# Optimization experiments

Hardware: AMD Instinct MI355X
Metric: run time of the kernel (lower is better)

## Reference

```python
import jax, jax.numpy as jnp
import numpy as np

N = 100_000
E = 1_600_000
H = 128
L = 3
EPS = 1e-5


def setup_inputs() -> dict:
    key = jax.random.key(0)
    ks = jax.random.split(key, 8)
    x = jax.random.normal(ks[0], (N, H), dtype=jnp.float32)
    edge_index = jax.random.randint(ks[1], (2, E), 0, N, dtype=jnp.int64)
    edge_weight = jax.random.uniform(ks[2], (E,), dtype=jnp.float32)
    # per-layer params (all layers are H->H since in_dim == hidden)
    s = 1.0 / np.sqrt(H)
    lin_neigh_w = jax.random.uniform(ks[3], (L, H, H), minval=-s, maxval=s, dtype=jnp.float32)
    lin_root_w = jax.random.uniform(ks[4], (L, H, H), minval=-s, maxval=s, dtype=jnp.float32)
    lin_root_b = jax.random.uniform(ks[5], (L, H), minval=-s, maxval=s, dtype=jnp.float32)
    ln_w = jnp.ones((L, H), dtype=jnp.float32)
    ln_b = jnp.zeros((L, H), dtype=jnp.float32)
    return {"x": x, "edge_index": edge_index, "edge_weight": edge_weight,
            "lin_neigh_w": lin_neigh_w, "lin_root_w": lin_root_w,
            "lin_root_b": lin_root_b, "ln_w": ln_w, "ln_b": ln_b}


def _layer(h, src, dst, e_w, w_neigh, w_root, b_root, g, b):
    # message: m_ij = w_ij * x_j ; aggregate: scatter-add over dst, normalized by sum of weights
    msg = e_w[:, None] * h[src]                                    # [E, H]
    agg = jax.ops.segment_sum(msg, dst, num_segments=N)            # [N, H]
    sum_w = jnp.clip(jax.ops.segment_sum(e_w, dst, num_segments=N), 1.0, None)
    out = agg / sum_w[:, None]
    out = out @ w_neigh.T + h @ w_root.T + b_root                  # lin_neigh + lin_root
    out = jax.nn.relu(out)
    # per-node LayerNorm over feature dim
    mu = jnp.mean(out, axis=-1, keepdims=True)
    var = jnp.var(out, axis=-1, keepdims=True)
    out = (out - mu) * jax.lax.rsqrt(var + EPS) * g + b
    return out  # dropout: inference no-op


def reference(x, edge_index, edge_weight, lin_neigh_w, lin_root_w, lin_root_b, ln_w, ln_b):
    src, dst = edge_index[0], edge_index[1]
    h = x
    for l in range(L):
        h = _layer(h, src, dst, edge_weight, lin_neigh_w[l], lin_root_w[l],
                   lin_root_b[l], ln_w[l], ln_b[l])
    return h
```

## Files before the change

### kernel.cpp

```cpp
#include <hip/hip_runtime.h>

#define H 128
#define EPS 1e-5f
#define BCAP 6144

typedef __attribute__((ext_vector_type(8))) short short8;
typedef __attribute__((ext_vector_type(4))) float f32x4;

__device__ inline unsigned short f2bf(float f) {
    unsigned u = __builtin_bit_cast(unsigned, f);
    unsigned r = (u + 0x7fff + ((u >> 16) & 1)) >> 16;
    return (unsigned short)r;
}
__device__ inline float bf2f_lo(unsigned u) { return __builtin_bit_cast(float, u << 16); }
__device__ inline float bf2f_hi(unsigned u) { return __builtin_bit_cast(float, u & 0xffff0000u); }

__global__ void convert_kernel(const float* __restrict__ x, unsigned* __restrict__ hx, int n4) {
    int i = blockIdx.x * 256 + threadIdx.x;
    if (i >= n4) return;
    float4 v = reinterpret_cast<const float4*>(x)[i];
    unsigned p0 = (unsigned)f2bf(v.x) | ((unsigned)f2bf(v.y) << 16);
    unsigned p1 = (unsigned)f2bf(v.z) | ((unsigned)f2bf(v.w) << 16);
    reinterpret_cast<uint2*>(hx)[i] = make_uint2(p0, p1);
}

__global__ __launch_bounds__(256) void bhist_kernel(const int* __restrict__ dst,
                                                    int* __restrict__ ghist, int E, int NB) {
    __shared__ int hist[512];
    int t = threadIdx.x;
    for (int i = t; i < NB; i += 256) hist[i] = 0;
    __syncthreads();
    int base = blockIdx.x * 8192 + t;
#pragma unroll
    for (int k = 0; k < 32; ++k) {
        int e = base + k * 256;
        if (e < E) atomicAdd(&hist[dst[e] >> 8], 1);
    }
    __syncthreads();
    for (int i = t; i < NB; i += 256)
        if (hist[i]) atomicAdd(&ghist[i], hist[i]);
}

__global__ __launch_bounds__(512) void bscan_kernel(const int* __restrict__ ghist,
                                                    int* __restrict__ bucket_base,
                                                    int* __restrict__ cursor,
                                                    int* __restrict__ row_start,
                                                    int NB, int E, int N) {
    __shared__ int lds[512];
    int t = threadIdx.x;
    int v = (t < NB) ? ghist[t] : 0;
    lds[t] = v;
    __syncthreads();
    for (int off = 1; off < 512; off <<= 1) {
        int u = (t >= off) ? lds[t - off] : 0;
        __syncthreads();
        lds[t] += u;
        __syncthreads();
    }
    int excl = lds[t] - v;
    if (t < NB) {
        bucket_base[t] = excl;
        cursor[t] = excl;
    }
    if (t == 0) {
        bucket_base[NB] = E;
        row_start[N] = E;
    }
}

__global__ __launch_bounds__(1024) void bucketize_kernel(const int* __restrict__ src,
                                                         const int* __restrict__ dst,
                                                         const float* __restrict__ ew,
                                                         int* __restrict__ cursor,
                                                         int2* __restrict__ ee, int E, int NB) {
    __shared__ int hist[512];
    __shared__ int scn[512];
    __shared__ int gbase[512];
    __shared__ int2 stage[8192];
    int t = threadIdx.x;
    for (int i = t; i < NB; i += 1024) hist[i] = 0;
    __syncthreads();

    int e0 = blockIdx.x * 8192;
    int bb[8], rk[8], pk[8], wb[8];
#pragma unroll
    for (int k = 0; k < 8; ++k) {
        int e = e0 + t + k * 1024;
        if (e < E) {
            int s = src[e], d = dst[e];
            bb[k] = d >> 8;
            pk[k] = s | ((d & 255) << 17);
            wb[k] = __float_as_int(ew[e]);
            rk[k] = atomicAdd(&hist[bb[k]], 1);
        } else {
            bb[k] = -1;
        }
    }
    __syncthreads();
    if (t < 512) scn[t] = (t < NB) ? hist[t] : 0;
    __syncthreads();
    for (int off = 1; off < 512; off <<= 1) {
        int u = 0;
        if (t < 512 && t >= off) u = scn[t - off];
        __syncthreads();
        if (t < 512) scn[t] += u;
        __syncthreads();
    }
    for (int i = t; i < NB; i += 1024) {
        int c = hist[i];
        if (c > 0) gbase[i] = atomicAdd(&cursor[i], c);
    }
#pragma unroll
    for (int k = 0; k < 8; ++k) {
        if (bb[k] >= 0) {
            int start = scn[bb[k]] - hist[bb[k]];
            stage[start + rk[k]] = make_int2(pk[k], wb[k]);
        }
    }
    __syncthreads();
    int wv = t >> 6, ln = t & 63;
    for (int bk = wv; bk < NB; bk += 16) {
        int c = hist[bk];
        if (c == 0) continue;
        int s0 = scn[bk] - c;
        int gb = gbase[bk];
        for (int i = ln; i < c; i += 64) ee[gb + i] = stage[s0 + i];
    }
}

__global__ __launch_bounds__(256) void bsort_kernel(int2* __restrict__ ee,
                                                    const int* __restrict__ bucket_base,
                                                    int* __restrict__ row_start, int N) {
    __shared__ int cnts[256];
    __shared__ int scv[256];
    __shared__ int prefs[256];
    __shared__ int2 out[BCAP];
    int b = blockIdx.x;
    int base = bucket_base[b], endb = bucket_base[b + 1];
    int cnt = endb - base;
    int t = threadIdx.x;
    cnts[t] = 0;
    __syncthreads();
    for (int i = base + t; i < endb; i += 256) atomicAdd(&cnts[(ee[i].x >> 17) & 255], 1);
    __syncthreads();
    scv[t] = cnts[t];
    __syncthreads();
    for (int off = 1; off < 256; off <<= 1) {
        int u = (t >= off) ? scv[t - off] : 0;
        __syncthreads();
        scv[t] += u;
        __syncthreads();
    }
    int pref = scv[t] - cnts[t];
    prefs[t] = pref;
    int node = (b << 8) + t;
    if (node < N) row_start[node] = base + pref;
    __syncthreads();
    cnts[t] = 0;
    __syncthreads();
    for (int i = base + t; i < endb; i += 256) {
        int2 r = ee[i];
        int dl = (r.x >> 17) & 255;
        int rkk = atomicAdd(&cnts[dl], 1);
        int slot = prefs[dl] + rkk;
        if (slot < BCAP) out[slot] = make_int2(r.x & 0x1FFFF, r.y);
    }
    __syncthreads();
    for (int i = t; i < cnt; i += 256) ee[base + i] = out[i];
}

__global__ __launch_bounds__(256) void agg_kernel(const unsigned short* __restrict__ hx,
                                                  const int* __restrict__ row_start,
                                                  const int2* __restrict__ ee,
                                                  unsigned short* __restrict__ aggb, int N) {
    int t = threadIdx.x;
    int node = blockIdx.x * 4 + (t >> 6);
    if (node >= N) return;
    int lane = t & 63, half = lane >> 5, jb = lane & 31;
    float a0 = 0.f, a1 = 0.f, a2 = 0.f, a3 = 0.f, sw = 0.f;
    int rs = row_start[node], re = row_start[node + 1];
    int i = rs + half;
    for (; i + 2 < re; i += 4) {
        int2 ea = ee[i], eb = ee[i + 2];
        uint2 ua = reinterpret_cast<const uint2*>(hx + (size_t)ea.x * H)[jb];
        uint2 ub = reinterpret_cast<const uint2*>(hx + (size_t)eb.x * H)[jb];
        float wa = __int_as_float(ea.y), wbv = __int_as_float(eb.y);
        a0 = fmaf(wa, bf2f_lo(ua.x), a0); a1 = fmaf(wa, bf2f_hi(ua.x), a1);
        a2 = fmaf(wa, bf2f_lo(ua.y), a2); a3 = fmaf(wa, bf2f_hi(ua.y), a3);
        a0 = fmaf(wbv, bf2f_lo(ub.x), a0); a1 = fmaf(wbv, bf2f_hi(ub.x), a1);
        a2 = fmaf(wbv, bf2f_lo(ub.y), a2); a3 = fmaf(wbv, bf2f_hi(ub.y), a3);
        sw += wa + wbv;
    }
    for (; i < re; i += 2) {
        int2 ea = ee[i];
        uint2 ua = reinterpret_cast<const uint2*>(hx + (size_t)ea.x * H)[jb];
        float wa = __int_as_float(ea.y);
        a0 = fmaf(wa, bf2f_lo(ua.x), a0); a1 = fmaf(wa, bf2f_hi(ua.x), a1);
        a2 = fmaf(wa, bf2f_lo(ua.y), a2); a3 = fmaf(wa, bf2f_hi(ua.y), a3);
        sw += wa;
    }
    a0 += __shfl_xor(a0, 32);
    a1 += __shfl_xor(a1, 32);
    a2 += __shfl_xor(a2, 32);
    a3 += __shfl_xor(a3, 32);
    sw += __shfl_xor(sw, 32);
    sw = sw < 1.f ? 1.f : sw;
    float inv = 1.f / sw;
    float fl = half ? a2 : a0;
    float fh = half ? a3 : a1;
    unsigned p = (unsigned)f2bf(fl * inv) | ((unsigned)f2bf(fh * inv) << 16);
    reinterpret_cast<unsigned*>(aggb + (size_t)node * H)[2 * jb + half] = p;
}

__global__ __launch_bounds__(256, 2) void gemm_ln_mfma(
    const unsigned short* __restrict__ aggb, const unsigned short* __restrict__ hx,
    const float* __restrict__ Wn, const float* __restrict__ Wr,
    const float* __restrict__ br, const float* __restrict__ g,
    const float* __restrict__ b, unsigned short* __restrict__ hout,
    float* __restrict__ outf, int final_layer, int N) {
    __shared__ short8 Bfl[4096];

    int t = threadIdx.x;
    int w = t >> 6, lane = t & 63;
    int Mbase = blockIdx.x * 256;

#pragma unroll
    for (int it = 0; it < 16; ++it) {
        int f = it * 4 + w;
        int kt = f >> 3, nb = f & 7;
        int n = nb * 16 + (lane & 15);
        int kk = (kt & 3) * 32 + (lane >> 4) * 8;
        const float* wp = ((kt < 4) ? Wn : Wr) + (size_t)n * H + kk;
        float4 wa = *reinterpret_cast<const float4*>(wp);
        float4 wb = *reinterpret_cast<const float4*>(wp + 4);
        short8 sv;
        sv[0] = (short)f2bf(wa.x); sv[1] = (short)f2bf(wa.y);
        sv[2] = (short)f2bf(wa.z); sv[3] = (short)f2bf(wa.w);
        sv[4] = (short)f2bf(wb.x); sv[5] = (short)f2bf(wb.y);
        sv[6] = (short)f2bf(wb.z); sv[7] = (short)f2bf(wb.w);
        Bfl[f * 64 + lane] = sv;
    }
    __syncthreads();

    int lrow = lane & 15, lk = lane >> 4;
    const char* aggp = (const char*)aggb;
    const char* hp = (const char*)hx;
    size_t rb[4];
#pragma unroll
    for (int mf = 0; mf < 4; ++mf) {
        int r = Mbase + w * 64 + mf * 16 + lrow;
        r = r < N ? r : N - 1;
        rb[mf] = (size_t)r * 256;
    }

    f32x4 acc[4][8];
#pragma unroll
    for (int mf = 0; mf < 4; ++mf)
#pragma unroll
        for (int nb = 0; nb < 8; ++nb) acc[mf][nb] = (f32x4){0.f, 0.f, 0.f, 0.f};

#pragma unroll
    for (int kt = 0; kt < 8; ++kt) {
        const char* base = (kt < 4) ? aggp : hp;
        int off = (kt & 3) * 64 + lk * 16;
        short8 bf[8];
#pragma unroll
        for (int nb = 0; nb < 8; ++nb) bf[nb] = Bfl[(kt * 8 + nb) * 64 + lane];
#pragma unroll
        for (int mf = 0; mf < 4; ++mf) {
            short8 av = *reinterpret_cast<const short8*>(base + rb[mf] + off);
#pragma unroll
            for (int nb = 0; nb < 8; ++nb)
                acc[mf][nb] = __builtin_amdgcn_mfma_f32_16x16x32_bf16(av, bf[nb], acc[mf][nb], 0, 0, 0);
        }
    }

    int col0 = lane & 15, rq = lane >> 4;
    float bias[8], gg[8], bbv[8];
#pragma unroll
    for (int nb = 0; nb < 8; ++nb) {
        int c = col0 + nb * 16;
        bias[nb] = br[c];
        gg[nb] = g[c];
        bbv[nb] = b[c];
    }
#pragma unroll
    for (int mf = 0; mf < 4; ++mf) {
#pragma unroll
        for (int reg = 0; reg < 4; ++reg) {
            float v[8];
            float s = 0.f, q = 0.f;
#pragma unroll
            for (int nb = 0; nb < 8; ++nb) {
                float u = acc[mf][nb][reg] + bias[nb];
                u = fmaxf(u, 0.f);
                v[nb] = u;
                s += u;
                q = fmaf(u, u, q);
            }
#pragma unroll
            for (int off = 1; off < 16; off <<= 1) {
                s += __shfl_xor(s, off);
                q += __shfl_xor(q, off);
            }
            float mu = s * (1.f / 128.f);
            float var = q * (1.f / 128.f) - mu * mu;
            float inv = rsqrtf(var + EPS);
            int grow = Mbase + w * 64 + mf * 16 + rq * 4 + reg;
            if (grow < N) {
                if (final_layer) {
#pragma unroll
                    for (int nb = 0; nb < 8; ++nb)
                        outf[(size_t)grow * H + col0 + nb * 16] = (v[nb] - mu) * inv * gg[nb] + bbv[nb];
                } else {
#pragma unroll
                    for (int nb = 0; nb < 8; ++nb)
                        hout[(size_t)grow * H + col0 + nb * 16] = f2bf((v[nb] - mu) * inv * gg[nb] + bbv[nb]);
                }
            }
        }
    }
}

static inline size_t alignup(size_t x) { return (x + 255) & ~(size_t)255; }

extern "C" void kernel_launch(void* const* d_in, const int* in_sizes, int n_in,
                              void* d_out, int out_size, void* d_ws, size_t ws_size,
                              hipStream_t stream) {
    const float* x  = (const float*)d_in[0];
    const int*   ei = (const int*)d_in[1];
    const float* ew = (const float*)d_in[2];
    const float* Wn = (const float*)d_in[3];
    const float* Wr = (const float*)d_in[4];
    const float* br = (const float*)d_in[5];
    const float* g  = (const float*)d_in[6];
    const float* bb = (const float*)d_in[7];
    float* out = (float*)d_out;

    int N = in_sizes[0] / H;
    int E = in_sizes[2];
    const int* src = ei;
    const int* dst = ei + E;
    int NB = (N + 255) >> 8;

    char* ws = (char*)d_ws;
    size_t off = 0;
    int* ghist = (int*)(ws + off);         off = alignup(off + sizeof(int) * 512);
    int* bucket_base = (int*)(ws + off);   off = alignup(off + sizeof(int) * 513);
    int* cursor = (int*)(ws + off);        off = alignup(off + sizeof(int) * 512);
    int* row_start = (int*)(ws + off);     off = alignup(off + sizeof(int) * ((size_t)N + 1));
    int2* ee = (int2*)(ws + off);          off = alignup(off + sizeof(int2) * (size_t)E);
    unsigned short* aggb = (unsigned short*)(ws + off); off = alignup(off + 2ull * N * H);
    unsigned short* hx = (unsigned short*)(ws + off);   off = alignup(off + 2ull * N * H);

    int eblocks = (E + 8191) / 8192;

    hipMemsetAsync(ghist, 0, sizeof(int) * 512, stream);
    bhist_kernel<<<eblocks, 256, 0, stream>>>(dst, ghist, E, NB);
    bscan_kernel<<<1, 512, 0, stream>>>(ghist, bucket_base, cursor, row_start, NB, E, N);
    bucketize_kernel<<<eblocks, 1024, 0, stream>>>(src, dst, ew, cursor, ee, E, NB);
    bsort_kernel<<<NB, 256, 0, stream>>>(ee, bucket_base, row_start, N);

    int n4 = N * H / 4;
    convert_kernel<<<(n4 + 255) / 256, 256, 0, stream>>>(x, (unsigned*)hx, n4);

    int gblocks = (N + 255) / 256;
    for (int l = 0; l < 3; ++l) {
        agg_kernel<<<(N + 3) / 4, 256, 0, stream>>>(hx, row_start, ee, aggb, N);
        gemm_ln_mfma<<<gblocks, 256, 0, stream>>>(
            aggb, hx,
            Wn + (size_t)l * H * H, Wr + (size_t)l * H * H, br + (size_t)l * H,
            g + (size_t)l * H, bb + (size_t)l * H,
            hx, out, (l == 2) ? 1 : 0, N);
    }
}
```

Before: 345.7 us.

## Switch activations to fp16 with packed half2 aggregation and prenormalized edge weights

Stores features in fp16 instead of bf16 and performs the neighbor aggregation with packed half2 FMAs, accumulating in fp16. Per-node weight-sum normalization moves into the CSR bucket-sort kernel, which writes each edge weight already divided by the clamped sum and duplicated as a half2. The aggregation loop is unrolled to four gathers per iteration, and the GEMM uses the f16 MFMA. This cuts conversion and FMA instruction count in the gather-bound aggregation, at the cost of fp16 accumulation error and overflow risk over many edges, plus a serial per-thread pass in the sort kernel.

```diff
diff --git a/kernel.cpp b/kernel.cpp
--- a/kernel.cpp
+++ b/kernel.cpp
@@ -1,26 +1,22 @@
 #include <hip/hip_runtime.h>
+#include <hip/hip_fp16.h>
 
 #define H 128
 #define EPS 1e-5f
 #define BCAP 6144
 
-typedef __attribute__((ext_vector_type(8))) short short8;
+typedef __attribute__((ext_vector_type(8))) _Float16 half8;
 typedef __attribute__((ext_vector_type(4))) float f32x4;
 
-__device__ inline unsigned short f2bf(float f) {
-    unsigned u = __builtin_bit_cast(unsigned, f);
-    unsigned r = (u + 0x7fff + ((u >> 16) & 1)) >> 16;
-    return (unsigned short)r;
-}
-__device__ inline float bf2f_lo(unsigned u) { return __builtin_bit_cast(float, u << 16); }
-__device__ inline float bf2f_hi(unsigned u) { return __builtin_bit_cast(float, u & 0xffff0000u); }
+__device__ inline __half2 u2h2(unsigned u) { return __builtin_bit_cast(__half2, u); }
+__device__ inline unsigned h22u(__half2 h) { return __builtin_bit_cast(unsigned, h); }
 
 __global__ void convert_kernel(const float* __restrict__ x, unsigned* __restrict__ hx, int n4) {
     int i = blockIdx.x * 256 + threadIdx.x;
     if (i >= n4) return;
     float4 v = reinterpret_cast<const float4*>(x)[i];
-    unsigned p0 = (unsigned)f2bf(v.x) | ((unsigned)f2bf(v.y) << 16);
-    unsigned p1 = (unsigned)f2bf(v.z) | ((unsigned)f2bf(v.w) << 16);
+    unsigned p0 = h22u(__floats2half2_rn(v.x, v.y));
+    unsigned p1 = h22u(__floats2half2_rn(v.z, v.w));
     reinterpret_cast<uint2*>(hx)[i] = make_uint2(p0, p1);
 }
 
@@ -166,6 +162,19 @@
         if (slot < BCAP) out[slot] = make_int2(r.x & 0x1FFFF, r.y);
     }
     __syncthreads();
+    {
+        int s0 = prefs[t], c = cnts[t];
+        float sw = 0.f;
+        for (int k = 0; k < c; ++k) sw += __int_as_float(out[s0 + k].y);
+        sw = sw < 1.f ? 1.f : sw;
+        float inv = 1.f / sw;
+        for (int k = 0; k < c; ++k) {
+            float w = __int_as_float(out[s0 + k].y) * inv;
+            unsigned hb = (unsigned)__half_as_ushort(__float2half(w));
+            out[s0 + k].y = (int)(hb | (hb << 16));
+        }
+    }
+    __syncthreads();
     for (int i = t; i < cnt; i += 256) ee[base + i] = out[i];
 }
 
@@ -177,38 +186,32 @@
     int node = blockIdx.x * 4 + (t >> 6);
     if (node >= N) return;
     int lane = t & 63, half = lane >> 5, jb = lane & 31;
-    float a0 = 0.f, a1 = 0.f, a2 = 0.f, a3 = 0.f, sw = 0.f;
+    __half2 a01 = u2h2(0), a23 = u2h2(0);
     int rs = row_start[node], re = row_start[node + 1];
     int i = rs + half;
-    for (; i + 2 < re; i += 4) {
-        int2 ea = ee[i], eb = ee[i + 2];
-        uint2 ua = reinterpret_cast<const uint2*>(hx + (size_t)ea.x * H)[jb];
-        uint2 ub = reinterpret_cast<const uint2*>(hx + (size_t)eb.x * H)[jb];
-        float wa = __int_as_float(ea.y), wbv = __int_as_float(eb.y);
-        a0 = fmaf(wa, bf2f_lo(ua.x), a0); a1 = fmaf(wa, bf2f_hi(ua.x), a1);
-        a2 = fmaf(wa, bf2f_lo(ua.y), a2); a3 = fmaf(wa, bf2f_hi(ua.y), a3);
-        a0 = fmaf(wbv, bf2f_lo(ub.x), a0); a1 = fmaf(wbv, bf2f_hi(ub.x), a1);
-        a2 = fmaf(wbv, bf2f_lo(ub.y), a2); a3 = fmaf(wbv, bf2f_hi(ub.y), a3);
-        sw += wa + wbv;
+    for (; i + 6 < re; i += 8) {
+        int2 e0 = ee[i], e1 = ee[i + 2], e2 = ee[i + 4], e3 = ee[i + 6];
+        uint2 u0 = reinterpret_cast<const uint2*>(hx + (size_t)e0.x * H)[jb];
+        uint2 u1 = reinterpret_cast<const uint2*>(hx + (size_t)e1.x * H)[jb];
+        uint2 u2 = reinterpret_cast<const uint2*>(hx + (size_t)e2.x * H)[jb];
+        uint2 u3 = reinterpret_cast<const uint2*>(hx + (size_t)e3.x * H)[jb];
+        __half2 w0 = u2h2((unsigned)e0.y), w1 = u2h2((unsigned)e1.y);
+        __half2 w2 = u2h2((unsigned)e2.y), w3 = u2h2((unsigned)e3.y);
+        a01 = __hfma2(u2h2(u0.x), w0, a01); a23 = __hfma2(u2h2(u0.y), w0, a23);
+        a01 = __hfma2(u2h2(u1.x), w1, a01); a23 = __hfma2(u2h2(u1.y), w1, a23);
+        a01 = __hfma2(u2h2(u2.x), w2, a01); a23 = __hfma2(u2h2(u2.y), w2, a23);
+        a01 = __hfma2(u2h2(u3.x), w3, a01); a23 = __hfma2(u2h2(u3.y), w3, a23);
     }
     for (; i < re; i += 2) {
-        int2 ea = ee[i];
-        uint2 ua = reinterpret_cast<const uint2*>(hx + (size_t)ea.x * H)[jb];
-        float wa = __int_as_float(ea.y);
-        a0 = fmaf(wa, bf2f_lo(ua.x), a0); a1 = fmaf(wa, bf2f_hi(ua.x), a1);
-        a2 = fmaf(wa, bf2f_lo(ua.y), a2); a3 = fmaf(wa, bf2f_hi(ua.y), a3);
-        sw += wa;
-    }
-    a0 += __shfl_xor(a0, 32);
-    a1 += __shfl_xor(a1, 32);
-    a2 += __shfl_xor(a2, 32);
-    a3 += __shfl_xor(a3, 32);
-    sw += __shfl_xor(sw, 32);
-    sw = sw < 1.f ? 1.f : sw;
-    float inv = 1.f / sw;
-    float fl = half ? a2 : a0;
-    float fh = half ? a3 : a1;
-    unsigned p = (unsigned)f2bf(fl * inv) | ((unsigned)f2bf(fh * inv) << 16);
+        int2 e0 = ee[i];
+        uint2 u0 = reinterpret_cast<const uint2*>(hx + (size_t)e0.x * H)[jb];
+        __half2 w0 = u2h2((unsigned)e0.y);
+        a01 = __hfma2(u2h2(u0.x), w0, a01);
+        a23 = __hfma2(u2h2(u0.y), w0, a23);
+    }
+    a01 = __hadd2(a01, u2h2((unsigned)__shfl_xor((int)h22u(a01), 32)));
+    a23 = __hadd2(a23, u2h2((unsigned)__shfl_xor((int)h22u(a23), 32)));
+    unsigned p = half ? h22u(a23) : h22u(a01);
     reinterpret_cast<unsigned*>(aggb + (size_t)node * H)[2 * jb + half] = p;
 }
 
@@ -218,7 +221,7 @@
     const float* __restrict__ br, const float* __restrict__ g,
     const float* __restrict__ b, unsigned short* __restrict__ hout,
     float* __restrict__ outf, int final_layer, int N) {
-    __shared__ short8 Bfl[4096];
+    __shared__ half8 Bfl[4096];
 
     int t = threadIdx.x;
     int w = t >> 6, lane = t & 63;
@@ -233,11 +236,11 @@
         const float* wp = ((kt < 4) ? Wn : Wr) + (size_t)n * H + kk;
         float4 wa = *reinterpret_cast<const float4*>(wp);
         float4 wb = *reinterpret_cast<const float4*>(wp + 4);
-        short8 sv;
-        sv[0] = (short)f2bf(wa.x); sv[1] = (short)f2bf(wa.y);
-        sv[2] = (short)f2bf(wa.z); sv[3] = (short)f2bf(wa.w);
-        sv[4] = (short)f2bf(wb.x); sv[5] = (short)f2bf(wb.y);
-        sv[6] = (short)f2bf(wb.z); sv[7] = (short)f2bf(wb.w);
+        half8 sv;
+        sv[0] = (_Float16)wa.x; sv[1] = (_Float16)wa.y;
+        sv[2] = (_Float16)wa.z; sv[3] = (_Float16)wa.w;
+        sv[4] = (_Float16)wb.x; sv[5] = (_Float16)wb.y;
+        sv[6] = (_Float16)wb.z; sv[7] = (_Float16)wb.w;
         Bfl[f * 64 + lane] = sv;
     }
     __syncthreads();
@@ -263,15 +266,15 @@
     for (int kt = 0; kt < 8; ++kt) {
         const char* base = (kt < 4) ? aggp : hp;
         int off = (kt & 3) * 64 + lk * 16;
-        short8 bf[8];
+        half8 bf[8];
 #pragma unroll
         for (int nb = 0; nb < 8; ++nb) bf[nb] = Bfl[(kt * 8 + nb) * 64 + lane];
 #pragma unroll
         for (int mf = 0; mf < 4; ++mf) {
-            short8 av = *reinterpret_cast<const short8*>(base + rb[mf] + off);
+            half8 av = *reinterpret_cast<const half8*>(base + rb[mf] + off);
 #pragma unroll
             for (int nb = 0; nb < 8; ++nb)
-                acc[mf][nb] = __builtin_amdgcn_mfma_f32_16x16x32_bf16(av, bf[nb], acc[mf][nb], 0, 0, 0);
+                acc[mf][nb] = __builtin_amdgcn_mfma_f32_16x16x32_f16(av, bf[nb], acc[mf][nb], 0, 0, 0);
         }
     }
 
@@ -315,7 +318,8 @@
                 } else {
 #pragma unroll
                     for (int nb = 0; nb < 8; ++nb)
-                        hout[(size_t)grow * H + col0 + nb * 16] = f2bf((v[nb] - mu) * inv * gg[nb] + bbv[nb]);
+                        hout[(size_t)grow * H + col0 + nb * 16] =
+                            __half_as_ushort(__float2half((v[nb] - mu) * inv * gg[nb] + bbv[nb]));
                 }
             }
         }
```

Result: faster. 333.5 us (-3.5%).
